# Optimization experiments

Hardware: AMD Instinct MI355X
Metric: run time of the kernel (lower is better)

The kernel has to match this reference:

```python
import jax, jax.numpy as jnp
import numpy as np
jax.config.update("jax_enable_x64", True)

N_ITER = 5
B, N = 64, 128

_C1 = jnp.uint64(0x9E3779B97F4A7C15)
_C2 = jnp.uint64(0xBF58476D1CE4E5B9)
_C3 = jnp.uint64(0x94D049BB133111EB)
_SALT = jnp.uint64(0xD1B54A32D192ED03)


def _mix(x):
    # splitmix64 finalizer: a bijection on uint64 -> preserves label equality classes
    z = x + _C1
    z = (z ^ (z >> jnp.uint64(30))) * _C2
    z = (z ^ (z >> jnp.uint64(27))) * _C3
    return z ^ (z >> jnp.uint64(31))


def setup_inputs() -> dict:
    key = jax.random.key(0)
    k1, k2 = jax.random.split(key)
    u = jax.random.uniform(k1, (B, N, N))
    adj = jnp.where(u < 0.06, 1.0, 0.0).astype(jnp.float32)
    adj = jnp.maximum(adj, jnp.transpose(adj, (0, 2, 1)))  # symmetric
    eye = jnp.eye(N, dtype=jnp.float32)
    adj = adj * (1.0 - eye)  # no self loops
    labels = jax.random.randint(k2, (B, N), 0, 10, dtype=jnp.int32)
    return {"adj": adj, "labels": labels}


def _kernel_contrib(h):
    # h: [B, N] uint64 labels. K[i,j] = #{(u,v): label_u == label_v}
    L = h.reshape(-1)                                   # [T]
    eq = (L[:, None] == L[None, :]).astype(jnp.float32)  # [T, T]
    return eq.reshape(B, N, B, N).sum(axis=(1, 3))       # [B, B]


def reference(adj, labels):
    adj_u = (adj > 0.5).astype(jnp.uint64)        # [B, N, N]
    h = _mix(labels.astype(jnp.uint64))           # initial labels (bijective relabel)
    K = _kernel_contrib(h)
    for _ in range(N_ITER):
        # commutative multiset hash of neighbor labels
        nsum = jnp.einsum('bij,bj->bi', adj_u, _mix(h ^ _SALT))
        # combine own label with neighbor multiset -> WL relabel
        h = _mix(_mix(h) + nsum)
        K = K + _kernel_contrib(h)
    d = jnp.sqrt(jnp.diag(K))
    return K / (d[:, None] * d[None, :])
```

## Files before the change

kernel.cpp:

```cpp
#include <hip/hip_runtime.h>

typedef unsigned long long u64;
typedef unsigned int u32;

#define NB 64
#define NN 128
#define NITER 5
#define NGEN 6
#define SALT 0xD1B54A32D192ED03ULL
#define NPAIR_OFF (NB*(NB-1)/2)

__device__ __forceinline__ u64 mix64(u64 x) {
    u64 z = x + 0x9E3779B97F4A7C15ULL;
    z = (z ^ (z >> 30)) * 0xBF58476D1CE4E5B9ULL;
    z = (z ^ (z >> 27)) * 0x94D049BB133111EBULL;
    return z ^ (z >> 31);
}

__global__ __launch_bounds__(512) void wl_propagate(const float* __restrict__ adj,
                                                    const int* __restrict__ labels,
                                                    u64* __restrict__ hgen,
                                                    float* __restrict__ Kdiag,
                                                    float* __restrict__ out) {
    const int b = blockIdx.x;
    const int t = threadIdx.x;
    const int wave = t >> 6;
    const int lane = t & 63;

    __shared__ u64 bits_sh[NN][2];
    __shared__ u64 h_sh[NN];
    __shared__ u64 g_sh[NN];
    __shared__ u64 hall[NGEN][NN];
    __shared__ u64 psum[4][NN];
    __shared__ u32 part[8];

    const float* abase = adj + (size_t)b * NN * NN;
    #pragma unroll 4
    for (int k = 0; k < 16; ++k) {
        const int row = wave * 16 + k;
        const float* arow = abase + (size_t)row * NN;
        u64 m0 = __ballot(arow[lane] > 0.5f);
        u64 m1 = __ballot(arow[64 + lane] > 0.5f);
        if (lane == 0) { bits_sh[row][0] = m0; bits_sh[row][1] = m1; }
    }

    if (t < NN) {
        u64 h = mix64((u64)(unsigned)labels[b * NN + t]);
        h_sh[t] = h;
        hall[0][t] = h;
        hgen[(size_t)b * (NGEN * NN) + t] = h;
    }
    __syncthreads();

    for (int it = 0; it < NITER; ++it) {
        if (t < NN) g_sh[t] = mix64(h_sh[t] ^ SALT);
        __syncthreads();
        {
            const int i = t & 127;
            const int q = t >> 7;
            u32 m = (u32)(bits_sh[i][q >> 1] >> ((q & 1) * 32));
            const u64* gp = g_sh + q * 32;
            u64 s = 0;
            while (m) {
                int j = __builtin_ctz(m);
                m &= m - 1;
                s += gp[j];
            }
            psum[q][i] = s;
        }
        __syncthreads();
        if (t < NN) {
            u64 hn = mix64(mix64(h_sh[t]) + psum[0][t] + psum[1][t] + psum[2][t] + psum[3][t]);
            h_sh[t] = hn;
            hall[it + 1][t] = hn;
            hgen[(size_t)b * (NGEN * NN) + (it + 1) * NN + t] = hn;
        }
        __syncthreads();
    }

    {
        const int i = t & 127;
        const int jq = t >> 7;
        u32 cnt = 0;
        for (int g = 0; g < NGEN; ++g) {
            const u64 a = hall[g][i];
            const u64* jp = &hall[g][jq * 32];
            #pragma unroll
            for (int jj = 0; jj < 32; ++jj) cnt += (a == jp[jj]) ? 1u : 0u;
        }
        #pragma unroll
        for (int off = 32; off > 0; off >>= 1) cnt += __shfl_down(cnt, off);
        if (lane == 0) part[wave] = cnt;
        __syncthreads();
        if (t == 0) {
            u32 d = 0;
            #pragma unroll
            for (int w = 0; w < 8; ++w) d += part[w];
            Kdiag[b] = (float)d;
            out[b * NB + b] = 1.0f;
        }
    }
}

__global__ __launch_bounds__(256) void wl_count(const u64* __restrict__ hgen,
                                                const float* __restrict__ Kdiag,
                                                float* __restrict__ out) {
    const int p = blockIdx.x;
    int b1 = (int)((1.0f + sqrtf(1.0f + 8.0f * (float)p)) * 0.5f);
    while (b1 * (b1 - 1) / 2 > p) --b1;
    while ((b1 + 1) * b1 / 2 <= p) ++b1;
    const int b2 = p - b1 * (b1 - 1) / 2;

    const int t = threadIdx.x;
    const int ag = t >> 3;
    const int bg = t & 7;

    __shared__ u64 Ash[NGEN][NN];
    __shared__ u64 Bsh[NGEN][NN];

    {
        const ulonglong2* sA = (const ulonglong2*)(hgen + (size_t)b1 * (NGEN * NN));
        const ulonglong2* sB = (const ulonglong2*)(hgen + (size_t)b2 * (NGEN * NN));
        ulonglong2* dA = (ulonglong2*)&Ash[0][0];
        ulonglong2* dB = (ulonglong2*)&Bsh[0][0];
        #pragma unroll
        for (int k = 0; k < 3; ++k) {
            const int idx = t + 256 * k;
            if (idx < 384) dA[idx] = sA[idx];
            else           dB[idx - 384] = sB[idx - 384];
        }
    }
    __syncthreads();

    u32 cnt = 0;
    for (int g = 0; g < NGEN; ++g) {
        const u64 a0 = Ash[g][ag * 4 + 0];
        const u64 a1 = Ash[g][ag * 4 + 1];
        const u64 a2 = Ash[g][ag * 4 + 2];
        const u64 a3 = Ash[g][ag * 4 + 3];
        const u64* Bp = &Bsh[g][bg * 16];
        #pragma unroll
        for (int jj = 0; jj < 8; ++jj) {
            const int idx = ((jj + bg) & 7) * 2;
            const u64 v0 = Bp[idx];
            const u64 v1 = Bp[idx + 1];
            cnt += (a0 == v0); cnt += (a0 == v1);
            cnt += (a1 == v0); cnt += (a1 == v1);
            cnt += (a2 == v0); cnt += (a2 == v1);
            cnt += (a3 == v0); cnt += (a3 == v1);
        }
    }

    #pragma unroll
    for (int off = 32; off > 0; off >>= 1) cnt += __shfl_down(cnt, off);
    __shared__ u32 part[4];
    if ((t & 63) == 0) part[t >> 6] = cnt;
    __syncthreads();
    if (t == 0) {
        const float v = (float)(part[0] + part[1] + part[2] + part[3])
                      / (sqrtf(Kdiag[b1]) * sqrtf(Kdiag[b2]));
        out[b1 * NB + b2] = v;
        out[b2 * NB + b1] = v;
    }
}

extern "C" void kernel_launch(void* const* d_in, const int* in_sizes, int n_in,
                              void* d_out, int out_size, void* d_ws, size_t ws_size,
                              hipStream_t stream) {
    const float* adj   = (const float*)d_in[0];
    const int*  labels = (const int*)d_in[1];
    float* out = (float*)d_out;

    u64*   hgen  = (u64*)d_ws;
    float* Kdiag = (float*)((char*)d_ws + (size_t)NB * NGEN * NN * 8);

    wl_propagate<<<NB, 512, 0, stream>>>(adj, labels, hgen, Kdiag, out);
    wl_count<<<NPAIR_OFF, 256, 0, stream>>>(hgen, Kdiag, out);
}
```

Measured before the change: 31.94 us.

## Replace all-pairs label comparison with per-graph shared-memory hash tables

Each graph builds, per WL generation, an open-addressing hash table in shared memory that maps each label to its count, using atomicCAS and atomicAdd. The diagonal kernel value is then a sum of squared counts. The pair kernel loads graph b2's tables from global memory and probes them with graph b1's labels, replacing the quadratic 128x128 compares per generation with roughly linear probes. This adds shared-memory atomics, a larger global workspace, and data-dependent probe loops that may diverge. It also assumes no label hashes to 0, since 0 marks an empty slot. The first loop is now fully unrolled.

```diff
diff --git a/kernel.cpp b/kernel.cpp
--- a/kernel.cpp
+++ b/kernel.cpp
@@ -9,6 +9,7 @@
 #define NGEN 6
 #define SALT 0xD1B54A32D192ED03ULL
 #define NPAIR_OFF (NB*(NB-1)/2)
+#define TSLOTS 256
 
 __device__ __forceinline__ u64 mix64(u64 x) {
     u64 z = x + 0x9E3779B97F4A7C15ULL;
@@ -17,9 +18,22 @@
     return z ^ (z >> 31);
 }
 
+__device__ __forceinline__ void tab_insert(ulonglong2* tab, u64 key) {
+    u32 s = (u32)key & (TSLOTS - 1);
+    for (;;) {
+        u64 old = atomicCAS((unsigned long long*)&tab[s].x, 0ULL, key);
+        if (old == 0ULL || old == key) {
+            atomicAdd((unsigned long long*)&tab[s].y, 1ULL);
+            return;
+        }
+        s = (s + 1) & (TSLOTS - 1);
+    }
+}
+
 __global__ __launch_bounds__(512) void wl_propagate(const float* __restrict__ adj,
                                                     const int* __restrict__ labels,
                                                     u64* __restrict__ hgen,
+                                                    ulonglong2* __restrict__ tabg,
                                                     float* __restrict__ Kdiag,
                                                     float* __restrict__ out) {
     const int b = blockIdx.x;
@@ -30,12 +44,12 @@
     __shared__ u64 bits_sh[NN][2];
     __shared__ u64 h_sh[NN];
     __shared__ u64 g_sh[NN];
-    __shared__ u64 hall[NGEN][NN];
     __shared__ u64 psum[4][NN];
+    __shared__ ulonglong2 tab[NGEN][TSLOTS];
     __shared__ u32 part[8];
 
     const float* abase = adj + (size_t)b * NN * NN;
-    #pragma unroll 4
+    #pragma unroll
     for (int k = 0; k < 16; ++k) {
         const int row = wave * 16 + k;
         const float* arow = abase + (size_t)row * NN;
@@ -44,13 +58,20 @@
         if (lane == 0) { bits_sh[row][0] = m0; bits_sh[row][1] = m1; }
     }
 
+    {
+        ulonglong2* tf = &tab[0][0];
+        #pragma unroll
+        for (int k = 0; k < 3; ++k) tf[t + 512 * k] = make_ulonglong2(0ULL, 0ULL);
+    }
+
     if (t < NN) {
         u64 h = mix64((u64)(unsigned)labels[b * NN + t]);
         h_sh[t] = h;
-        hall[0][t] = h;
         hgen[(size_t)b * (NGEN * NN) + t] = h;
     }
     __syncthreads();
+
+    if (t < NN) tab_insert(tab[0], h_sh[t]);
 
     for (int it = 0; it < NITER; ++it) {
         if (t < NN) g_sh[t] = mix64(h_sh[t] ^ SALT);
@@ -72,25 +93,26 @@
         if (t < NN) {
             u64 hn = mix64(mix64(h_sh[t]) + psum[0][t] + psum[1][t] + psum[2][t] + psum[3][t]);
             h_sh[t] = hn;
-            hall[it + 1][t] = hn;
             hgen[(size_t)b * (NGEN * NN) + (it + 1) * NN + t] = hn;
+            tab_insert(tab[it + 1], hn);
         }
         __syncthreads();
     }
 
     {
-        const int i = t & 127;
-        const int jq = t >> 7;
-        u32 cnt = 0;
-        for (int g = 0; g < NGEN; ++g) {
-            const u64 a = hall[g][i];
-            const u64* jp = &hall[g][jq * 32];
-            #pragma unroll
-            for (int jj = 0; jj < 32; ++jj) cnt += (a == jp[jj]) ? 1u : 0u;
+        const ulonglong2* tf = &tab[0][0];
+        ulonglong2* tg = tabg + (size_t)b * (NGEN * TSLOTS);
+        u32 acc = 0;
+        #pragma unroll
+        for (int k = 0; k < 3; ++k) {
+            const ulonglong2 v = tf[t + 512 * k];
+            tg[t + 512 * k] = v;
+            const u32 c = (u32)v.y;
+            acc += c * c;
         }
         #pragma unroll
-        for (int off = 32; off > 0; off >>= 1) cnt += __shfl_down(cnt, off);
-        if (lane == 0) part[wave] = cnt;
+        for (int off = 32; off > 0; off >>= 1) acc += __shfl_down(acc, off);
+        if (lane == 0) part[wave] = acc;
         __syncthreads();
         if (t == 0) {
             u32 d = 0;
@@ -102,7 +124,8 @@
     }
 }
 
-__global__ __launch_bounds__(256) void wl_count(const u64* __restrict__ hgen,
+__global__ __launch_bounds__(256) void wl_pairs(const u64* __restrict__ hgen,
+                                                const ulonglong2* __restrict__ tabg,
                                                 const float* __restrict__ Kdiag,
                                                 float* __restrict__ out) {
     const int p = blockIdx.x;
@@ -112,42 +135,28 @@
     const int b2 = p - b1 * (b1 - 1) / 2;
 
     const int t = threadIdx.x;
-    const int ag = t >> 3;
-    const int bg = t & 7;
-
-    __shared__ u64 Ash[NGEN][NN];
-    __shared__ u64 Bsh[NGEN][NN];
+    __shared__ ulonglong2 tab[NGEN * TSLOTS];
 
     {
-        const ulonglong2* sA = (const ulonglong2*)(hgen + (size_t)b1 * (NGEN * NN));
-        const ulonglong2* sB = (const ulonglong2*)(hgen + (size_t)b2 * (NGEN * NN));
-        ulonglong2* dA = (ulonglong2*)&Ash[0][0];
-        ulonglong2* dB = (ulonglong2*)&Bsh[0][0];
+        const ulonglong2* src = tabg + (size_t)b2 * (NGEN * TSLOTS);
         #pragma unroll
-        for (int k = 0; k < 3; ++k) {
-            const int idx = t + 256 * k;
-            if (idx < 384) dA[idx] = sA[idx];
-            else           dB[idx - 384] = sB[idx - 384];
-        }
+        for (int k = 0; k < 6; ++k) tab[t + 256 * k] = src[t + 256 * k];
     }
     __syncthreads();
 
     u32 cnt = 0;
-    for (int g = 0; g < NGEN; ++g) {
-        const u64 a0 = Ash[g][ag * 4 + 0];
-        const u64 a1 = Ash[g][ag * 4 + 1];
-        const u64 a2 = Ash[g][ag * 4 + 2];
-        const u64 a3 = Ash[g][ag * 4 + 3];
-        const u64* Bp = &Bsh[g][bg * 16];
-        #pragma unroll
-        for (int jj = 0; jj < 8; ++jj) {
-            const int idx = ((jj + bg) & 7) * 2;
-            const u64 v0 = Bp[idx];
-            const u64 v1 = Bp[idx + 1];
-            cnt += (a0 == v0); cnt += (a0 == v1);
-            cnt += (a1 == v0); cnt += (a1 == v1);
-            cnt += (a2 == v0); cnt += (a2 == v1);
-            cnt += (a3 == v0); cnt += (a3 == v1);
+    const u64* abase = hgen + (size_t)b1 * (NGEN * NN);
+    #pragma unroll
+    for (int k = 0; k < 3; ++k) {
+        const int idx = t + 256 * k;
+        const u64 a = abase[idx];
+        const ulonglong2* tg = tab + (idx >> 7) * TSLOTS;
+        u32 s = (u32)a & (TSLOTS - 1);
+        for (;;) {
+            const ulonglong2 v = tg[s];
+            if (v.x == a) { cnt += (u32)v.y; break; }
+            if (v.x == 0ULL) break;
+            s = (s + 1) & (TSLOTS - 1);
         }
     }
 
@@ -171,9 +180,11 @@
     const int*  labels = (const int*)d_in[1];
     float* out = (float*)d_out;
 
-    u64*   hgen  = (u64*)d_ws;
-    float* Kdiag = (float*)((char*)d_ws + (size_t)NB * NGEN * NN * 8);
+    char* ws = (char*)d_ws;
+    u64*        hgen  = (u64*)ws;
+    float*      Kdiag = (float*)(ws + 448 * 1024);
+    ulonglong2* tabg  = (ulonglong2*)(ws + 512 * 1024);
 
-    wl_propagate<<<NB, 512, 0, stream>>>(adj, labels, hgen, Kdiag, out);
-    wl_count<<<NPAIR_OFF, 256, 0, stream>>>(hgen, Kdiag, out);
+    wl_propagate<<<NB, 512, 0, stream>>>(adj, labels, hgen, tabg, Kdiag, out);
+    wl_pairs<<<NPAIR_OFF, 256, 0, stream>>>(hgen, tabg, Kdiag, out);
 }
```

Measured after the change: 32.33 us. No clear change (+1.2%).
